# Kernel optimization log

Hardware: AMD Instinct MI355X
Metric: run time of the kernel (lower is better)

## Reference

```python
import jax, jax.numpy as jnp
import numpy as np

INPUT_SIZE = 128
OUTPUT_SIZE = 32
LIFTING_DIM = 512
BATCH = 32768


def setup_inputs() -> dict:
    key = jax.random.key(0)
    ks = jax.random.split(key, 7)
    x = jax.random.normal(ks[0], (BATCH, INPUT_SIZE), dtype=jnp.float32)
    # Linear(input_size, lifting_dim) with bias (torch layout: W [out, in])
    lim1 = 1.0 / np.sqrt(INPUT_SIZE)
    W1 = jax.random.uniform(ks[1], (LIFTING_DIM, INPUT_SIZE), jnp.float32, -lim1, lim1)
    b1 = jax.random.uniform(ks[2], (LIFTING_DIM,), jnp.float32, -lim1, lim1)
    # Linear(lifting_dim, output_size, bias=False)
    lim2 = 1.0 / np.sqrt(LIFTING_DIM)
    W2 = jax.random.uniform(ks[3], (OUTPUT_SIZE, LIFTING_DIM), jnp.float32, -lim2, lim2)
    # Quadratic params: L_vars ~ randn, b ~ randn, c ~ randn (as in module init)
    n_tril = LIFTING_DIM * (LIFTING_DIM + 1) // 2
    L_vars = jax.random.normal(ks[4], (n_tril,), dtype=jnp.float32)
    qb = jax.random.normal(ks[5], (LIFTING_DIM,), dtype=jnp.float32)
    qc = jax.random.normal(ks[6], (1,), dtype=jnp.float32)
    return {"x": x, "W1": W1, "b1": b1, "W2": W2, "L_vars": L_vars, "qb": qb, "qc": qc}


def reference(x, W1, b1, W2, L_vars, qb, qc):
    # lifting: phi = tanh(x @ W1^T + b1)   [B, lifting_dim]
    phi = jnp.tanh(x @ W1.T + b1)
    # actor: linear feedback (no bias)     [B, output_size]
    pi = phi @ W2.T
    # critic: quadratic form y = phi' Q phi + b' phi + c with Q = L L^T (PSD)
    rows, cols = jnp.tril_indices(LIFTING_DIM)  # row-major, same order as torch.tril_indices
    L = jnp.zeros((LIFTING_DIM, LIFTING_DIM), dtype=L_vars.dtype).at[rows, cols].set(L_vars)
    Q = L @ L.T
    # diag(phi @ Q @ phi.T) == sum((phi @ Q) * phi, axis=1)  -- O(B*d^2), same math
    y = jnp.sum((phi @ Q) * phi, axis=1) + phi @ qb + qc  # [B]
    vf = y[:, None]  # [B, 1]
    return pi, vf
```

## Files before the change

### kernel.cpp

```cpp
#include <hip/hip_runtime.h>
#include <hip/hip_bf16.h>
#include <stdint.h>

typedef short bf16x8 __attribute__((ext_vector_type(8)));
typedef float f32x4 __attribute__((ext_vector_type(4)));
typedef float f32x16 __attribute__((ext_vector_type(16)));

#define DEVI static __device__ __forceinline__

constexpr int B_   = 32768;
constexpr int IN_  = 128;
constexpr int LF_  = 512;
constexpr int OUT_ = 32;

constexpr size_t OFF_LTF = 0;
constexpr size_t OFF_W1F = 524288;
constexpr size_t OFF_W2F = OFF_W1F + 131072;

DEVI short f2bs(float f) { __hip_bfloat16 h = __float2bfloat16(f); return *(short*)&h; }

DEVI float tanh_fast(float v) {
    float e = __expf(2.0f * v);
    return 1.0f - 2.0f * __builtin_amdgcn_rcpf(e + 1.0f);
}

DEVI bf16x8 fragGL(const __hip_bfloat16* base, int chunk, int ln) {
    return *(const bf16x8*)(base + ((size_t)chunk * 64 + ln) * 8);
}
DEVI f32x16 mfma32(bf16x8 a, bf16x8 b, f32x16 c) {
    return __builtin_amdgcn_mfma_f32_32x32x16_bf16(a, b, c, 0, 0, 0);
}

DEVI bf16x8 phiFrag(const char* p, int row, int kofs) {
    int c = (kofs >> 3) ^ (row & 7);
    return *(const bf16x8*)(p + (size_t)((row << 6) + c) * 16);
}
DEVI bf16x8 phiFrag32(const char* p, int h, int ks, int ln) {
    int row = h * 32 + (ln & 31);
    int c = (ks * 2 + (ln >> 5)) ^ (row & 7);
    return *(const bf16x8*)(p + (size_t)((row << 6) + c) * 16);
}
DEVI bf16x8 xFrag(const char* p, int row, int kofs) {
    int c = (kofs >> 3) ^ (row & 15);
    return *(const bf16x8*)(p + (size_t)((row << 4) + c) * 16);
}

template <int WV>
DEVI void p3loops(const char* phiB, const __hip_bfloat16* ltf, int ln,
                  f32x16 acc[2][2]) {
    constexpr int T1 = 15 - WV;
#pragma unroll
    for (int ks = 2 * WV; ks < 2 * T1; ++ks) {
        bf16x8 b0 = fragGL(ltf, WV * 32 + ks, ln);
        bf16x8 a0 = phiFrag32(phiB, 0, ks, ln);
        bf16x8 a1 = phiFrag32(phiB, 1, ks, ln);
        acc[0][0] = mfma32(a0, b0, acc[0][0]);
        acc[0][1] = mfma32(a1, b0, acc[0][1]);
    }
#pragma unroll
    for (int ks = 2 * T1; ks < 32; ++ks) {
        bf16x8 b0 = fragGL(ltf, WV * 32 + ks, ln);
        bf16x8 b1 = fragGL(ltf, T1 * 32 + ks, ln);
        bf16x8 a0 = phiFrag32(phiB, 0, ks, ln);
        bf16x8 a1 = phiFrag32(phiB, 1, ks, ln);
        acc[0][0] = mfma32(a0, b0, acc[0][0]);
        acc[0][1] = mfma32(a1, b0, acc[0][1]);
        acc[1][0] = mfma32(a0, b1, acc[1][0]);
        acc[1][1] = mfma32(a1, b1, acc[1][1]);
    }
}

__global__ __launch_bounds__(256) void k_prep(
        const float* __restrict__ w1, const float* __restrict__ w2,
        const float* __restrict__ lv, const float* __restrict__ qb,
        __hip_bfloat16* __restrict__ w1f, __hip_bfloat16* __restrict__ w2f,
        __hip_bfloat16* __restrict__ ltf) {
    int cid = blockIdx.x * 256 + threadIdx.x;
    if (cid < 8192) {
        int ln = cid & 63, ks = (cid >> 6) & 3, nt = cid >> 8;
        int n = nt * 16 + (ln & 15), kb = ks * 32 + (ln >> 4) * 8;
        const float* src = w1 + (size_t)n * IN_ + kb;
        bf16x8 o;
#pragma unroll
        for (int i = 0; i < 8; ++i) o[i] = f2bs(src[i]);
        *(bf16x8*)(w1f + (size_t)cid * 8) = o;
    } else if (cid < 11264) {
        int c2 = cid - 8192;
        int ln = c2 & 63, ks = (c2 >> 6) & 15, nt = c2 >> 10;
        int n = nt * 16 + (ln & 15), kb = ks * 32 + (ln >> 4) * 8;
        bf16x8 o;
#pragma unroll
        for (int i = 0; i < 8; ++i) {
            float v = (n < OUT_) ? w2[(size_t)n * LF_ + kb + i]
                                 : (n == OUT_ ? qb[kb + i] : 0.f);
            o[i] = f2bs(v);
        }
        *(bf16x8*)(w2f + (size_t)c2 * 8) = o;
    } else if (cid < 44032) {
        int c3 = cid - 11264;
        int ln = c3 & 63, ks = (c3 >> 6) & 31, t = c3 >> 11;
        int n = t * 32 + (ln & 31), kb = ks * 16 + (ln >> 5) * 8;
        bf16x8 o;
#pragma unroll
        for (int i = 0; i < 8; ++i) {
            int k = kb + i;
            o[i] = (k >= n) ? f2bs(lv[(size_t)k * (k + 1) / 2 + n]) : (short)0;
        }
        *(bf16x8*)(ltf + (size_t)c3 * 8) = o;
    }
}

__global__ __launch_bounds__(512, 4) void k_fused(
        const float* __restrict__ x, const __hip_bfloat16* __restrict__ w1f,
        const float* __restrict__ b1, const __hip_bfloat16* __restrict__ w2f,
        const __hip_bfloat16* __restrict__ ltf, const float* __restrict__ qcp,
        float* __restrict__ pi, float* __restrict__ vf) {
    __shared__ char smem[81920];
    char*  phiB  = smem;
    char*  stage = smem + 65536;
    float* vfb   = (float*)stage;
    float* vfp   = (float*)(stage + 256);

    const int tid = threadIdx.x, wv = tid >> 6, ln = tid & 63;
    const int cl = ln & 15, q = ln >> 4;
    const int m0 = blockIdx.x * 64;

#pragma unroll
    for (int it = 0; it < 2; ++it) {
        int slot = it * 512 + tid, row = slot >> 4, cg = slot & 15;
        const float4* p = (const float4*)(x + (size_t)(m0 + row) * IN_ + cg * 8);
        float4 u0 = p[0], u1 = p[1];
        bf16x8 pk;
        pk[0] = f2bs(u0.x); pk[1] = f2bs(u0.y); pk[2] = f2bs(u0.z); pk[3] = f2bs(u0.w);
        pk[4] = f2bs(u1.x); pk[5] = f2bs(u1.y); pk[6] = f2bs(u1.z); pk[7] = f2bs(u1.w);
        *(bf16x8*)(stage + (size_t)((row << 4) + (cg ^ (row & 15))) * 16) = pk;
    }
    __syncthreads();

    {
        f32x4 acc[4][4] = {};
#pragma unroll
        for (int ks = 0; ks < 4; ++ks) {
            bf16x8 a[4], wfr[4];
#pragma unroll
            for (int mi = 0; mi < 4; ++mi) a[mi] = xFrag(stage, mi * 16 + cl, ks * 32 + q * 8);
#pragma unroll
            for (int ni = 0; ni < 4; ++ni) wfr[ni] = fragGL(w1f, (4 * wv + ni) * 4 + ks, ln);
#pragma unroll
            for (int ni = 0; ni < 4; ++ni)
#pragma unroll
                for (int mi = 0; mi < 4; ++mi)
                    acc[ni][mi] = __builtin_amdgcn_mfma_f32_16x16x32_bf16(
                        wfr[ni], a[mi], acc[ni][mi], 0, 0, 0);
        }
#pragma unroll
        for (int ni = 0; ni < 4; ++ni) {
            float4 bb = *(const float4*)(b1 + wv * 64 + ni * 16 + q * 4);
            int c0 = wv * 8 + ni * 2 + (q >> 1);
#pragma unroll
            for (int mi = 0; mi < 4; ++mi) {
                int row = mi * 16 + cl;
                short4 pk;
                pk.x = f2bs(tanh_fast(acc[ni][mi][0] + bb.x));
                pk.y = f2bs(tanh_fast(acc[ni][mi][1] + bb.y));
                pk.z = f2bs(tanh_fast(acc[ni][mi][2] + bb.z));
                pk.w = f2bs(tanh_fast(acc[ni][mi][3] + bb.w));
                *(short4*)(phiB + (size_t)((row << 6) + (c0 ^ (row & 7))) * 16
                           + (q & 1) * 8) = pk;
            }
        }
    }
    __syncthreads();

    {
        int ids[2] = { (wv < 4) ? 2 * wv : 8 + (wv - 4), (wv < 4) ? 2 * wv + 1 : -1 };
#pragma unroll
        for (int u = 0; u < 2; ++u) {
            int id = ids[u];
            if (id < 0) continue;
            int mi = id & 3, ni = id >> 2;
            f32x4 a2 = {};
#pragma unroll
            for (int ks = 0; ks < 16; ++ks) {
                bf16x8 a = phiFrag(phiB, mi * 16 + cl, ks * 32 + q * 8);
                bf16x8 b = fragGL(w2f, ni * 16 + ks, ln);
                a2 = __builtin_amdgcn_mfma_f32_16x16x32_bf16(a, b, a2, 0, 0, 0);
            }
#pragma unroll
            for (int r = 0; r < 4; ++r) {
                int row = mi * 16 + q * 4 + r, col = ni * 16 + cl;
                if (col < OUT_)       pi[(size_t)(m0 + row) * OUT_ + col] = a2[r];
                else if (col == OUT_) vfb[row] = a2[r];
            }
        }
    }

    {
        f32x16 acc[2][2] = {};
        switch (wv) {
            case 0: p3loops<0>(phiB, ltf, ln, acc); break;
            case 1: p3loops<1>(phiB, ltf, ln, acc); break;
            case 2: p3loops<2>(phiB, ltf, ln, acc); break;
            case 3: p3loops<3>(phiB, ltf, ln, acc); break;
            case 4: p3loops<4>(phiB, ltf, ln, acc); break;
            case 5: p3loops<5>(phiB, ltf, ln, acc); break;
            case 6: p3loops<6>(phiB, ltf, ln, acc); break;
            default: p3loops<7>(phiB, ltf, ln, acc); break;
        }
#pragma unroll
        for (int h = 0; h < 2; ++h)
#pragma unroll
            for (int r = 0; r < 16; ++r) {
                float t0 = acc[0][h][r], t1 = acc[1][h][r];
                float s = t0 * t0 + t1 * t1;
                s += __shfl_xor(s, 1, 64);
                s += __shfl_xor(s, 2, 64);
                s += __shfl_xor(s, 4, 64);
                s += __shfl_xor(s, 8, 64);
                s += __shfl_xor(s, 16, 64);
                if ((ln & 31) == 0)
                    vfp[wv * 64 + h * 32 + (r & 3) + 8 * (r >> 2) + 4 * (ln >> 5)] = s;
            }
    }
    __syncthreads();
    if (tid < 64) {
        float v = vfb[tid] + qcp[0];
#pragma unroll
        for (int w = 0; w < 8; ++w) v += vfp[w * 64 + tid];
        vf[m0 + tid] = v;
    }
}

extern "C" void kernel_launch(void* const* d_in, const int* in_sizes, int n_in,
                              void* d_out, int out_size, void* d_ws, size_t ws_size,
                              hipStream_t stream) {
    const float* x  = (const float*)d_in[0];
    const float* w1 = (const float*)d_in[1];
    const float* b1 = (const float*)d_in[2];
    const float* w2 = (const float*)d_in[3];
    const float* lv = (const float*)d_in[4];
    const float* qb = (const float*)d_in[5];
    const float* qc = (const float*)d_in[6];

    char* ws = (char*)d_ws;
    __hip_bfloat16* ltf = (__hip_bfloat16*)(ws + OFF_LTF);
    __hip_bfloat16* w1f = (__hip_bfloat16*)(ws + OFF_W1F);
    __hip_bfloat16* w2f = (__hip_bfloat16*)(ws + OFF_W2F);

    float* pi = (float*)d_out;
    float* vf = pi + (size_t)B_ * OUT_;

    k_prep <<<172, 256, 0, stream>>>(w1, w2, lv, qb, w1f, w2f, ltf);
    k_fused<<<B_ / 64, 512, 0, stream>>>(x, w1f, b1, w2f, ltf, qc, pi, vf);
}
```

Before: 108.7 us.

## Split fused kernel into phi kernel and pi/quadratic kernel via global MFMA-layout slab

Splits the single fused kernel into two: one computes phi = tanh(xW1+b1) and writes it to a global workspace in a fragment-ordered bf16 layout, and a second loads that slab into LDS with direct global-to-LDS loads and runs the pi and quadratic-form GEMMs. The goal is lower LDS use and register pressure per kernel, which should raise occupancy, and conflict-free contiguous fragment reads in place of swizzled ones. In exchange it adds a 32 MB round trip through global memory for phi and an extra kernel launch.

```diff
diff --git a/kernel.cpp b/kernel.cpp
--- a/kernel.cpp
+++ b/kernel.cpp
@@ -16,6 +16,7 @@
 constexpr size_t OFF_LTF = 0;
 constexpr size_t OFF_W1F = 524288;
 constexpr size_t OFF_W2F = OFF_W1F + 131072;
+constexpr size_t OFF_PHI = OFF_W2F + 49152;
 
 DEVI short f2bs(float f) { __hip_bfloat16 h = __float2bfloat16(f); return *(short*)&h; }
 
@@ -24,6 +25,13 @@
     return 1.0f - 2.0f * __builtin_amdgcn_rcpf(e + 1.0f);
 }
 
+DEVI void gl2lds16(const void* g, void* l) {
+    __builtin_amdgcn_global_load_lds(
+        (const __attribute__((address_space(1))) unsigned int*)g,
+        (__attribute__((address_space(3))) unsigned int*)l,
+        16, 0, 0);
+}
+
 DEVI bf16x8 fragGL(const __hip_bfloat16* base, int chunk, int ln) {
     return *(const bf16x8*)(base + ((size_t)chunk * 64 + ln) * 8);
 }
@@ -31,18 +39,14 @@
     return __builtin_amdgcn_mfma_f32_32x32x16_bf16(a, b, c, 0, 0, 0);
 }
 
-DEVI bf16x8 phiFrag(const char* p, int row, int kofs) {
-    int c = (kofs >> 3) ^ (row & 7);
-    return *(const bf16x8*)(p + (size_t)((row << 6) + c) * 16);
-}
-DEVI bf16x8 phiFrag32(const char* p, int h, int ks, int ln) {
-    int row = h * 32 + (ln & 31);
-    int c = (ks * 2 + (ln >> 5)) ^ (row & 7);
-    return *(const bf16x8*)(p + (size_t)((row << 6) + c) * 16);
-}
 DEVI bf16x8 xFrag(const char* p, int row, int kofs) {
     int c = (kofs >> 3) ^ (row & 15);
     return *(const bf16x8*)(p + (size_t)((row << 4) + c) * 16);
+}
+DEVI bf16x8 phi16(const char* p, int mi, int ks, int cl, int q) {
+    int chunk = ks * 4 + (q >> 1) * 2 + (mi >> 1);
+    int slot  = (mi & 1) * 16 + cl + 32 * (q & 1);
+    return *(const bf16x8*)(p + ((size_t)chunk * 64 + slot) * 16);
 }
 
 template <int WV>
@@ -52,8 +56,8 @@
 #pragma unroll
     for (int ks = 2 * WV; ks < 2 * T1; ++ks) {
         bf16x8 b0 = fragGL(ltf, WV * 32 + ks, ln);
-        bf16x8 a0 = phiFrag32(phiB, 0, ks, ln);
-        bf16x8 a1 = phiFrag32(phiB, 1, ks, ln);
+        bf16x8 a0 = *(const bf16x8*)(phiB + (size_t)(ks * 2 + 0) * 1024 + (size_t)ln * 16);
+        bf16x8 a1 = *(const bf16x8*)(phiB + (size_t)(ks * 2 + 1) * 1024 + (size_t)ln * 16);
         acc[0][0] = mfma32(a0, b0, acc[0][0]);
         acc[0][1] = mfma32(a1, b0, acc[0][1]);
     }
@@ -61,8 +65,8 @@
     for (int ks = 2 * T1; ks < 32; ++ks) {
         bf16x8 b0 = fragGL(ltf, WV * 32 + ks, ln);
         bf16x8 b1 = fragGL(ltf, T1 * 32 + ks, ln);
-        bf16x8 a0 = phiFrag32(phiB, 0, ks, ln);
-        bf16x8 a1 = phiFrag32(phiB, 1, ks, ln);
+        bf16x8 a0 = *(const bf16x8*)(phiB + (size_t)(ks * 2 + 0) * 1024 + (size_t)ln * 16);
+        bf16x8 a1 = *(const bf16x8*)(phiB + (size_t)(ks * 2 + 1) * 1024 + (size_t)ln * 16);
         acc[0][0] = mfma32(a0, b0, acc[0][0]);
         acc[0][1] = mfma32(a1, b0, acc[0][1]);
         acc[1][0] = mfma32(a0, b1, acc[1][0]);
@@ -110,17 +114,10 @@
     }
 }
 
-__global__ __launch_bounds__(512, 4) void k_fused(
+__global__ __launch_bounds__(512, 4) void k_phi(
         const float* __restrict__ x, const __hip_bfloat16* __restrict__ w1f,
-        const float* __restrict__ b1, const __hip_bfloat16* __restrict__ w2f,
-        const __hip_bfloat16* __restrict__ ltf, const float* __restrict__ qcp,
-        float* __restrict__ pi, float* __restrict__ vf) {
-    __shared__ char smem[81920];
-    char*  phiB  = smem;
-    char*  stage = smem + 65536;
-    float* vfb   = (float*)stage;
-    float* vfp   = (float*)(stage + 256);
-
+        const float* __restrict__ b1, __hip_bfloat16* __restrict__ phig) {
+    __shared__ char stage[16384];
     const int tid = threadIdx.x, wv = tid >> 6, ln = tid & 63;
     const int cl = ln & 15, q = ln >> 4;
     const int m0 = blockIdx.x * 64;
@@ -137,38 +134,57 @@
     }
     __syncthreads();
 
-    {
-        f32x4 acc[4][4] = {};
-#pragma unroll
-        for (int ks = 0; ks < 4; ++ks) {
-            bf16x8 a[4], wfr[4];
-#pragma unroll
-            for (int mi = 0; mi < 4; ++mi) a[mi] = xFrag(stage, mi * 16 + cl, ks * 32 + q * 8);
-#pragma unroll
-            for (int ni = 0; ni < 4; ++ni) wfr[ni] = fragGL(w1f, (4 * wv + ni) * 4 + ks, ln);
-#pragma unroll
-            for (int ni = 0; ni < 4; ++ni)
-#pragma unroll
-                for (int mi = 0; mi < 4; ++mi)
-                    acc[ni][mi] = __builtin_amdgcn_mfma_f32_16x16x32_bf16(
-                        wfr[ni], a[mi], acc[ni][mi], 0, 0, 0);
-        }
-#pragma unroll
-        for (int ni = 0; ni < 4; ++ni) {
-            float4 bb = *(const float4*)(b1 + wv * 64 + ni * 16 + q * 4);
-            int c0 = wv * 8 + ni * 2 + (q >> 1);
-#pragma unroll
-            for (int mi = 0; mi < 4; ++mi) {
-                int row = mi * 16 + cl;
-                short4 pk;
-                pk.x = f2bs(tanh_fast(acc[ni][mi][0] + bb.x));
-                pk.y = f2bs(tanh_fast(acc[ni][mi][1] + bb.y));
-                pk.z = f2bs(tanh_fast(acc[ni][mi][2] + bb.z));
-                pk.w = f2bs(tanh_fast(acc[ni][mi][3] + bb.w));
-                *(short4*)(phiB + (size_t)((row << 6) + (c0 ^ (row & 7))) * 16
-                           + (q & 1) * 8) = pk;
-            }
-        }
+    f32x4 acc[4][4] = {};
+#pragma unroll
+    for (int ks = 0; ks < 4; ++ks) {
+        bf16x8 a[4], wfr[4];
+#pragma unroll
+        for (int mi = 0; mi < 4; ++mi) a[mi] = xFrag(stage, mi * 16 + cl, ks * 32 + q * 8);
+#pragma unroll
+        for (int ni = 0; ni < 4; ++ni) wfr[ni] = fragGL(w1f, (4 * wv + ni) * 4 + ks, ln);
+#pragma unroll
+        for (int ni = 0; ni < 4; ++ni)
+#pragma unroll
+            for (int mi = 0; mi < 4; ++mi)
+                acc[ni][mi] = __builtin_amdgcn_mfma_f32_16x16x32_bf16(
+                    wfr[ni], a[mi], acc[ni][mi], 0, 0, 0);
+    }
+    __hip_bfloat16* slab = phig + (size_t)blockIdx.x * 32768;
+#pragma unroll
+    for (int ni = 0; ni < 4; ++ni) {
+        float4 bb = *(const float4*)(b1 + wv * 64 + ni * 16 + q * 4);
+#pragma unroll
+        for (int mi = 0; mi < 4; ++mi) {
+            short4 pk;
+            pk.x = f2bs(tanh_fast(acc[ni][mi][0] + bb.x));
+            pk.y = f2bs(tanh_fast(acc[ni][mi][1] + bb.y));
+            pk.z = f2bs(tanh_fast(acc[ni][mi][2] + bb.z));
+            pk.w = f2bs(tanh_fast(acc[ni][mi][3] + bb.w));
+            size_t idx = (size_t)((wv * 4 + ni) * 2 + (mi >> 1)) * 512
+                       + ((mi & 1) * 16 + cl + 32 * (q >> 1)) * 8 + (q & 1) * 4;
+            *(short4*)(slab + idx) = pk;
+        }
+    }
+}
+
+__global__ __launch_bounds__(512, 4) void k_piy(
+        const __hip_bfloat16* __restrict__ phig, const __hip_bfloat16* __restrict__ w2f,
+        const __hip_bfloat16* __restrict__ ltf, const float* __restrict__ qcp,
+        float* __restrict__ pi, float* __restrict__ vf) {
+    __shared__ char smem[67840];
+    char*  phiB = smem;
+    float* vfb  = (float*)(smem + 65536);
+    float* vfp  = (float*)(smem + 65792);
+
+    const int tid = threadIdx.x, wv = tid >> 6, ln = tid & 63;
+    const int cl = ln & 15, q = ln >> 4;
+    const int m0 = blockIdx.x * 64;
+    const __hip_bfloat16* slab = phig + (size_t)blockIdx.x * 32768;
+
+#pragma unroll
+    for (int r = 0; r < 8; ++r) {
+        int c = (r * 8 + wv) * 64;
+        gl2lds16(slab + ((size_t)c + ln) * 8, phiB + (size_t)c * 16);
     }
     __syncthreads();
 
@@ -182,7 +198,7 @@
             f32x4 a2 = {};
 #pragma unroll
             for (int ks = 0; ks < 16; ++ks) {
-                bf16x8 a = phiFrag(phiB, mi * 16 + cl, ks * 32 + q * 8);
+                bf16x8 a = phi16(phiB, mi, ks, cl, q);
                 bf16x8 b = fragGL(w2f, ni * 16 + ks, ln);
                 a2 = __builtin_amdgcn_mfma_f32_16x16x32_bf16(a, b, a2, 0, 0, 0);
             }
@@ -243,13 +259,15 @@
     const float* qc = (const float*)d_in[6];
 
     char* ws = (char*)d_ws;
-    __hip_bfloat16* ltf = (__hip_bfloat16*)(ws + OFF_LTF);
-    __hip_bfloat16* w1f = (__hip_bfloat16*)(ws + OFF_W1F);
-    __hip_bfloat16* w2f = (__hip_bfloat16*)(ws + OFF_W2F);
+    __hip_bfloat16* ltf  = (__hip_bfloat16*)(ws + OFF_LTF);
+    __hip_bfloat16* w1f  = (__hip_bfloat16*)(ws + OFF_W1F);
+    __hip_bfloat16* w2f  = (__hip_bfloat16*)(ws + OFF_W2F);
+    __hip_bfloat16* phig = (__hip_bfloat16*)(ws + OFF_PHI);
 
     float* pi = (float*)d_out;
     float* vf = pi + (size_t)B_ * OUT_;
 
-    k_prep <<<172, 256, 0, stream>>>(w1, w2, lv, qb, w1f, w2f, ltf);
-    k_fused<<<B_ / 64, 512, 0, stream>>>(x, w1f, b1, w2f, ltf, qc, pi, vf);
-}
+    k_prep<<<172, 256, 0, stream>>>(w1, w2, lv, qb, w1f, w2f, ltf);
+    k_phi <<<B_ / 64, 512, 0, stream>>>(x, w1f, b1, phig);
+    k_piy <<<B_ / 64, 512, 0, stream>>>(phig, w2f, ltf, qc, pi, vf);
+}
```

After: 116.0 us. 6.8% more time.

## Pipeline phi computation in K-slices with double-buffered LDS across stages

Applied to the files above, without the earlier changes.

The kernel no longer computes the whole 512-wide phi tile into a 64KB LDS buffer before the actor and critic GEMMs. It now produces phi in four 128-column slices into two 16KB ping-pong buffers, and consumes each previous slice for the W2 and L-factor MFMAs while the next slice is being produced. This cuts LDS use from 80KB to about 50KB, which can raise blocks per CU, and overlaps the tanh/phase-1 work with the later MFMA work. In exchange it adds four barriers and runtime triangular-skip branches, since the per-wave template specialisation is gone. It also keeps more accumulators live at once, which raises register pressure.

```diff
diff --git a/kernel.cpp b/kernel.cpp
--- a/kernel.cpp
+++ b/kernel.cpp
@@ -30,44 +30,21 @@
 DEVI f32x16 mfma32(bf16x8 a, bf16x8 b, f32x16 c) {
     return __builtin_amdgcn_mfma_f32_32x32x16_bf16(a, b, c, 0, 0, 0);
 }
-
-DEVI bf16x8 phiFrag(const char* p, int row, int kofs) {
-    int c = (kofs >> 3) ^ (row & 7);
-    return *(const bf16x8*)(p + (size_t)((row << 6) + c) * 16);
-}
-DEVI bf16x8 phiFrag32(const char* p, int h, int ks, int ln) {
-    int row = h * 32 + (ln & 31);
-    int c = (ks * 2 + (ln >> 5)) ^ (row & 7);
-    return *(const bf16x8*)(p + (size_t)((row << 6) + c) * 16);
-}
+DEVI f32x4 mfma16(bf16x8 a, bf16x8 b, f32x4 c) {
+    return __builtin_amdgcn_mfma_f32_16x16x32_bf16(a, b, c, 0, 0, 0);
+}
+
 DEVI bf16x8 xFrag(const char* p, int row, int kofs) {
     int c = (kofs >> 3) ^ (row & 15);
     return *(const bf16x8*)(p + (size_t)((row << 4) + c) * 16);
 }
-
-template <int WV>
-DEVI void p3loops(const char* phiB, const __hip_bfloat16* ltf, int ln,
-                  f32x16 acc[2][2]) {
-    constexpr int T1 = 15 - WV;
-#pragma unroll
-    for (int ks = 2 * WV; ks < 2 * T1; ++ks) {
-        bf16x8 b0 = fragGL(ltf, WV * 32 + ks, ln);
-        bf16x8 a0 = phiFrag32(phiB, 0, ks, ln);
-        bf16x8 a1 = phiFrag32(phiB, 1, ks, ln);
-        acc[0][0] = mfma32(a0, b0, acc[0][0]);
-        acc[0][1] = mfma32(a1, b0, acc[0][1]);
-    }
-#pragma unroll
-    for (int ks = 2 * T1; ks < 32; ++ks) {
-        bf16x8 b0 = fragGL(ltf, WV * 32 + ks, ln);
-        bf16x8 b1 = fragGL(ltf, T1 * 32 + ks, ln);
-        bf16x8 a0 = phiFrag32(phiB, 0, ks, ln);
-        bf16x8 a1 = phiFrag32(phiB, 1, ks, ln);
-        acc[0][0] = mfma32(a0, b0, acc[0][0]);
-        acc[0][1] = mfma32(a1, b0, acc[0][1]);
-        acc[1][0] = mfma32(a0, b1, acc[1][0]);
-        acc[1][1] = mfma32(a1, b1, acc[1][1]);
-    }
+DEVI bf16x8 phi16s(const char* p, int mi, int ksl, int cl, int q) {
+    int chunk = ksl * 4 + (q >> 1) * 2 + (mi >> 1);
+    int slot  = (mi & 1) * 16 + cl + 32 * (q & 1);
+    return *(const bf16x8*)(p + ((size_t)chunk * 64 + slot) * 16);
+}
+DEVI bf16x8 phi32s(const char* p, int i16, int h, int ln) {
+    return *(const bf16x8*)(p + ((size_t)(i16 * 2 + h) * 64 + ln) * 16);
 }
 
 __global__ __launch_bounds__(256) void k_prep(
@@ -115,15 +92,22 @@
         const float* __restrict__ b1, const __hip_bfloat16* __restrict__ w2f,
         const __hip_bfloat16* __restrict__ ltf, const float* __restrict__ qcp,
         float* __restrict__ pi, float* __restrict__ vf) {
-    __shared__ char smem[81920];
-    char*  phiB  = smem;
-    char*  stage = smem + 65536;
-    float* vfb   = (float*)stage;
-    float* vfp   = (float*)(stage + 256);
+    __shared__ char smem[51456];
+    char*  xs   = smem;
+    char*  bufA = smem + 16384;
+    char*  bufB = smem + 32768;
+    float* vfb  = (float*)(smem + 49152);
+    float* vfp  = (float*)(smem + 49408);
 
     const int tid = threadIdx.x, wv = tid >> 6, ln = tid & 63;
     const int cl = ln & 15, q = ln >> 4;
     const int m0 = blockIdx.x * 64;
+    const int T1 = 15 - wv;
+    const int id0 = (wv < 4) ? 2 * wv : 8 + (wv - 4);
+    const int id1 = (wv < 4) ? 2 * wv + 1 : -1;
+
+    f32x16 acc3[2][2] = {};
+    f32x4  acc2[2]    = {{0,0,0,0},{0,0,0,0}};
 
 #pragma unroll
     for (int it = 0; it < 2; ++it) {
@@ -133,95 +117,135 @@
         bf16x8 pk;
         pk[0] = f2bs(u0.x); pk[1] = f2bs(u0.y); pk[2] = f2bs(u0.z); pk[3] = f2bs(u0.w);
         pk[4] = f2bs(u1.x); pk[5] = f2bs(u1.y); pk[6] = f2bs(u1.z); pk[7] = f2bs(u1.w);
-        *(bf16x8*)(stage + (size_t)((row << 4) + (cg ^ (row & 15))) * 16) = pk;
+        *(bf16x8*)(xs + (size_t)((row << 4) + (cg ^ (row & 15))) * 16) = pk;
     }
     __syncthreads();
 
+#pragma unroll
+    for (int s = 0; s < 4; ++s) {
+        char* wbuf = (s & 1) ? bufB : bufA;
+        char* rbuf = (s & 1) ? bufA : bufB;
+
+        {
+            f32x4 p1a[4] = {};
+#pragma unroll
+            for (int ks = 0; ks < 4; ++ks) {
+                bf16x8 wfr = fragGL(w1f, (s * 8 + wv) * 4 + ks, ln);
+#pragma unroll
+                for (int mi = 0; mi < 4; ++mi) {
+                    bf16x8 a = xFrag(xs, mi * 16 + cl, ks * 32 + q * 8);
+                    p1a[mi] = mfma16(wfr, a, p1a[mi]);
+                }
+            }
+            float4 bb = *(const float4*)(b1 + s * 128 + wv * 16 + q * 4);
+#pragma unroll
+            for (int mi = 0; mi < 4; ++mi) {
+                int m = mi * 16 + cl;
+                short4 pk;
+                pk.x = f2bs(tanh_fast(p1a[mi][0] + bb.x));
+                pk.y = f2bs(tanh_fast(p1a[mi][1] + bb.y));
+                pk.z = f2bs(tanh_fast(p1a[mi][2] + bb.z));
+                pk.w = f2bs(tanh_fast(p1a[mi][3] + bb.w));
+                *(short4*)(wbuf + (((size_t)(wv * 2 + (mi >> 1)) * 64
+                            + (m & 31) + 32 * (q >> 1)) * 16) + (q & 1) * 8) = pk;
+            }
+        }
+
+        if (s > 0) {
+            const int sp = s - 1;
+#pragma unroll
+            for (int i = 0; i < 8; ++i) {
+                const int ks = sp * 8 + i;
+                bool t0 = (ks >= 2 * wv), t1 = (ks >= 2 * T1);
+                if (t0) {
+                    bf16x8 a0 = phi32s(rbuf, i, 0, ln);
+                    bf16x8 a1 = phi32s(rbuf, i, 1, ln);
+                    bf16x8 b0 = fragGL(ltf, wv * 32 + ks, ln);
+                    acc3[0][0] = mfma32(a0, b0, acc3[0][0]);
+                    acc3[0][1] = mfma32(a1, b0, acc3[0][1]);
+                    if (t1) {
+                        bf16x8 b1f = fragGL(ltf, T1 * 32 + ks, ln);
+                        acc3[1][0] = mfma32(a0, b1f, acc3[1][0]);
+                        acc3[1][1] = mfma32(a1, b1f, acc3[1][1]);
+                    }
+                }
+            }
+#pragma unroll
+            for (int u = 0; u < 2; ++u) {
+                int id = (u == 0) ? id0 : id1;
+                if (id >= 0) {
+                    int mi = id & 3, ni = id >> 2;
+#pragma unroll
+                    for (int ksl = 0; ksl < 4; ++ksl) {
+                        bf16x8 a = phi16s(rbuf, mi, ksl, cl, q);
+                        bf16x8 b = fragGL(w2f, ni * 16 + sp * 4 + ksl, ln);
+                        acc2[u] = mfma16(a, b, acc2[u]);
+                    }
+                }
+            }
+        }
+        __syncthreads();
+    }
+
     {
-        f32x4 acc[4][4] = {};
-#pragma unroll
-        for (int ks = 0; ks < 4; ++ks) {
-            bf16x8 a[4], wfr[4];
-#pragma unroll
-            for (int mi = 0; mi < 4; ++mi) a[mi] = xFrag(stage, mi * 16 + cl, ks * 32 + q * 8);
-#pragma unroll
-            for (int ni = 0; ni < 4; ++ni) wfr[ni] = fragGL(w1f, (4 * wv + ni) * 4 + ks, ln);
-#pragma unroll
-            for (int ni = 0; ni < 4; ++ni)
-#pragma unroll
-                for (int mi = 0; mi < 4; ++mi)
-                    acc[ni][mi] = __builtin_amdgcn_mfma_f32_16x16x32_bf16(
-                        wfr[ni], a[mi], acc[ni][mi], 0, 0, 0);
-        }
-#pragma unroll
-        for (int ni = 0; ni < 4; ++ni) {
-            float4 bb = *(const float4*)(b1 + wv * 64 + ni * 16 + q * 4);
-            int c0 = wv * 8 + ni * 2 + (q >> 1);
-#pragma unroll
-            for (int mi = 0; mi < 4; ++mi) {
-                int row = mi * 16 + cl;
-                short4 pk;
-                pk.x = f2bs(tanh_fast(acc[ni][mi][0] + bb.x));
-                pk.y = f2bs(tanh_fast(acc[ni][mi][1] + bb.y));
-                pk.z = f2bs(tanh_fast(acc[ni][mi][2] + bb.z));
-                pk.w = f2bs(tanh_fast(acc[ni][mi][3] + bb.w));
-                *(short4*)(phiB + (size_t)((row << 6) + (c0 ^ (row & 7))) * 16
-                           + (q & 1) * 8) = pk;
-            }
-        }
-    }
-    __syncthreads();
-
-    {
-        int ids[2] = { (wv < 4) ? 2 * wv : 8 + (wv - 4), (wv < 4) ? 2 * wv + 1 : -1 };
+        const int sp = 3;
+#pragma unroll
+        for (int i = 0; i < 8; ++i) {
+            const int ks = sp * 8 + i;
+            bool t1 = (ks >= 2 * T1);
+            bf16x8 a0 = phi32s(bufB, i, 0, ln);
+            bf16x8 a1 = phi32s(bufB, i, 1, ln);
+            bf16x8 b0 = fragGL(ltf, wv * 32 + ks, ln);
+            acc3[0][0] = mfma32(a0, b0, acc3[0][0]);
+            acc3[0][1] = mfma32(a1, b0, acc3[0][1]);
+            if (t1) {
+                bf16x8 b1f = fragGL(ltf, T1 * 32 + ks, ln);
+                acc3[1][0] = mfma32(a0, b1f, acc3[1][0]);
+                acc3[1][1] = mfma32(a1, b1f, acc3[1][1]);
+            }
+        }
 #pragma unroll
         for (int u = 0; u < 2; ++u) {
-            int id = ids[u];
-            if (id < 0) continue;
+            int id = (u == 0) ? id0 : id1;
+            if (id >= 0) {
+                int mi = id & 3, ni = id >> 2;
+#pragma unroll
+                for (int ksl = 0; ksl < 4; ++ksl) {
+                    bf16x8 a = phi16s(bufB, mi, ksl, cl, q);
+                    bf16x8 b = fragGL(w2f, ni * 16 + sp * 4 + ksl, ln);
+                    acc2[u] = mfma16(a, b, acc2[u]);
+                }
+            }
+        }
+    }
+
+#pragma unroll
+    for (int u = 0; u < 2; ++u) {
+        int id = (u == 0) ? id0 : id1;
+        if (id >= 0) {
             int mi = id & 3, ni = id >> 2;
-            f32x4 a2 = {};
-#pragma unroll
-            for (int ks = 0; ks < 16; ++ks) {
-                bf16x8 a = phiFrag(phiB, mi * 16 + cl, ks * 32 + q * 8);
-                bf16x8 b = fragGL(w2f, ni * 16 + ks, ln);
-                a2 = __builtin_amdgcn_mfma_f32_16x16x32_bf16(a, b, a2, 0, 0, 0);
-            }
 #pragma unroll
             for (int r = 0; r < 4; ++r) {
                 int row = mi * 16 + q * 4 + r, col = ni * 16 + cl;
-                if (col < OUT_)       pi[(size_t)(m0 + row) * OUT_ + col] = a2[r];
-                else if (col == OUT_) vfb[row] = a2[r];
-            }
-        }
-    }
-
-    {
-        f32x16 acc[2][2] = {};
-        switch (wv) {
-            case 0: p3loops<0>(phiB, ltf, ln, acc); break;
-            case 1: p3loops<1>(phiB, ltf, ln, acc); break;
-            case 2: p3loops<2>(phiB, ltf, ln, acc); break;
-            case 3: p3loops<3>(phiB, ltf, ln, acc); break;
-            case 4: p3loops<4>(phiB, ltf, ln, acc); break;
-            case 5: p3loops<5>(phiB, ltf, ln, acc); break;
-            case 6: p3loops<6>(phiB, ltf, ln, acc); break;
-            default: p3loops<7>(phiB, ltf, ln, acc); break;
-        }
-#pragma unroll
-        for (int h = 0; h < 2; ++h)
-#pragma unroll
-            for (int r = 0; r < 16; ++r) {
-                float t0 = acc[0][h][r], t1 = acc[1][h][r];
-                float s = t0 * t0 + t1 * t1;
-                s += __shfl_xor(s, 1, 64);
-                s += __shfl_xor(s, 2, 64);
-                s += __shfl_xor(s, 4, 64);
-                s += __shfl_xor(s, 8, 64);
-                s += __shfl_xor(s, 16, 64);
-                if ((ln & 31) == 0)
-                    vfp[wv * 64 + h * 32 + (r & 3) + 8 * (r >> 2) + 4 * (ln >> 5)] = s;
-            }
-    }
+                if (col < OUT_)       pi[(size_t)(m0 + row) * OUT_ + col] = acc2[u][r];
+                else if (col == OUT_) vfb[row] = acc2[u][r];
+            }
+        }
+    }
+#pragma unroll
+    for (int h = 0; h < 2; ++h)
+#pragma unroll
+        for (int r = 0; r < 16; ++r) {
+            float t0 = acc3[0][h][r], t1 = acc3[1][h][r];
+            float s = t0 * t0 + t1 * t1;
+            s += __shfl_xor(s, 1, 64);
+            s += __shfl_xor(s, 2, 64);
+            s += __shfl_xor(s, 4, 64);
+            s += __shfl_xor(s, 8, 64);
+            s += __shfl_xor(s, 16, 64);
+            if ((ln & 31) == 0)
+                vfp[wv * 64 + h * 32 + (r & 3) + 8 * (r >> 2) + 4 * (ln >> 5)] = s;
+        }
     __syncthreads();
     if (tid < 64) {
         float v = vfb[tid] + qcp[0];
```

After: 114.2 us. 5.1% more time.
